# Kernel tuning notes

Measured on AMD Instinct MI355X. Metric: run time of the kernel, lower is better.

The kernel has to match this reference:

```python
import jax, jax.numpy as jnp
import numpy as np

N_NODES = 100000
N_EDGES = 1600000
HIDDEN = 256
CONV_OUT = 128
OUT = 2


def setup_inputs() -> dict:
    key = jax.random.key(0)
    k1, k2, k3, k4, k5, k6, k7 = jax.random.split(key, 7)
    x = jax.random.normal(k1, (N_NODES, HIDDEN), dtype=jnp.float32)
    edge_index = jax.random.randint(k2, (2, N_EDGES), 0, N_NODES, dtype=jnp.int64)
    edge_weight = jax.random.uniform(k3, (N_EDGES,), dtype=jnp.float32)
    # GCNConv parameters (lin: hidden->128, bias added after aggregation)
    W1 = jax.random.normal(k4, (HIDDEN, CONV_OUT), dtype=jnp.float32) / np.sqrt(HIDDEN)
    b1 = jnp.zeros((CONV_OUT,), dtype=jnp.float32)
    # head Linear(128, out_channels)
    W2 = jax.random.normal(k5, (CONV_OUT, OUT), dtype=jnp.float32) / np.sqrt(CONV_OUT)
    b2 = jax.random.normal(k6, (OUT,), dtype=jnp.float32) * 0.01
    return {"x": x, "edge_index": edge_index, "edge_weight": edge_weight,
            "W1": W1, "b1": b1, "W2": W2, "b2": b2}


def reference(x, edge_index, edge_weight, W1, b1, W2, b2):
    # GCNConv (use_weights=True branch, no relu), dropout in eval mode (identity), then Linear.
    N = x.shape[0]
    src, dst = edge_index[0], edge_index[1]
    # add self-loops with weight 1 (PyG default fill_value=1.0)
    loop = jnp.arange(N, dtype=src.dtype)
    src = jnp.concatenate([src, loop])
    dst = jnp.concatenate([dst, loop])
    w = jnp.concatenate([edge_weight, jnp.ones((N,), dtype=edge_weight.dtype)])
    # symmetric normalization: norm = d^{-1/2}[src] * w * d^{-1/2}[dst]
    deg = jax.ops.segment_sum(w, dst, num_segments=N)
    dinv = jnp.where(deg > 0, jax.lax.rsqrt(deg), 0.0)
    norm = dinv[src] * w * dinv[dst]
    # transform then gather-scatter aggregate
    h = x @ W1                                   # [N, 128]
    msgs = norm[:, None] * h[src]                # [E+N, 128]
    agg = jax.ops.segment_sum(msgs, dst, num_segments=N) + b1  # [N, 128]
    return agg @ W2 + b2                         # [N, out_channels]
```

## Files before the change

### kernel.cpp

```cpp
#include <hip/hip_runtime.h>

#define N_NODES 100000
#define N_EDGES 1600000
#define HIDDEN 256

#define BSH 7
#define BNODES 128
#define NB 782
#define NPB 256
#define EPB 6250
#define SLOTS 32
#define NZB 1563


__global__ __launch_bounds__(1024) void k_place(
        const int* __restrict__ ei, const float* __restrict__ ew,
        const float* __restrict__ W1, const float* __restrict__ b1,
        const float* __restrict__ W2, const float* __restrict__ b2,
        int* __restrict__ cnt, uint2* __restrict__ rec,
        float* __restrict__ W12, float* __restrict__ cvec) {
    const int tid = threadIdx.x, bid = blockIdx.x;
    if (bid == NPB) {
        if (tid < HIDDEN) {
            const float4* w1r = (const float4*)(W1 + (size_t)tid * 128);
            float a0 = 0.f, a1 = 0.f;
#pragma unroll 8
            for (int k4 = 0; k4 < 32; ++k4) {
                float4 v = w1r[k4];
                a0 += v.x * W2[8 * k4 + 0]; a1 += v.x * W2[8 * k4 + 1];
                a0 += v.y * W2[8 * k4 + 2]; a1 += v.y * W2[8 * k4 + 3];
                a0 += v.z * W2[8 * k4 + 4]; a1 += v.z * W2[8 * k4 + 5];
                a0 += v.w * W2[8 * k4 + 6]; a1 += v.w * W2[8 * k4 + 7];
            }
            W12[2 * tid] = a0; W12[2 * tid + 1] = a1;
            if (tid < 2) {
                float acc = b2[tid];
                for (int k = 0; k < 128; ++k) acc += b1[k] * W2[2 * k + tid];
                cvec[tid] = acc;
            }
        }
        return;
    }
    __shared__ int cursor[NB];
    for (int i = tid; i < NB; i += 1024) cursor[i] = 0;
    __syncthreads();
    const int e0 = bid * EPB, e1 = e0 + EPB;
    for (int e = e0 + tid; e < e1; e += 1024) {
        int d = ei[N_EDGES + e];
        int s = ei[e];
        float wv = ew[e];
        int bk = ((unsigned)d) >> BSH;
        int pos = atomicAdd(&cursor[bk], 1);
        if (pos < SLOTS)
            rec[((size_t)bk * NPB + bid) * SLOTS + pos] =
                make_uint2((unsigned)s | ((unsigned)(d & (BNODES - 1)) << 17),
                           __float_as_uint(wv));
    }
    __syncthreads();
    for (int i = tid; i < NB; i += 1024)
        cnt[(size_t)i * NPB + bid] = min(cursor[i], SLOTS);
}

__global__ __launch_bounds__(256) void k_zdeg(
        const float* __restrict__ x, const float* __restrict__ W12,
        const uint2* __restrict__ rec, const int* __restrict__ cnt,
        float* __restrict__ z, float* __restrict__ dinv) {
    __shared__ float acc[BNODES];
    const int tid = threadIdx.x, bid = blockIdx.x;
    if (bid < NZB) {
        const int lane = tid & 63;
        const int sub  = lane & 15;
        const int nid  = lane >> 4;
        float w0r[16], w1r[16];
#pragma unroll
        for (int j = 0; j < 16; ++j) {
            float2 wp = ((const float2*)W12)[sub * 16 + j];
            w0r[j] = wp.x; w1r[j] = wp.y;
        }
        const int base = bid * 64 + (tid >> 6) * 16;
#pragma unroll
        for (int k = 0; k < 4; ++k) {
            const int node = base + k * 4 + nid;
            if (node < N_NODES) {
                const float* xp = x + (size_t)node * HIDDEN + sub * 16;
                float xa[16];
                *(float4*)(xa + 0)  = *(const float4*)(xp + 0);
                *(float4*)(xa + 4)  = *(const float4*)(xp + 4);
                *(float4*)(xa + 8)  = *(const float4*)(xp + 8);
                *(float4*)(xa + 12) = *(const float4*)(xp + 12);
                float a0 = 0.f, a1 = 0.f;
#pragma unroll
                for (int j = 0; j < 16; ++j) {
                    a0 += xa[j] * w0r[j];
                    a1 += xa[j] * w1r[j];
                }
#pragma unroll
                for (int m = 1; m <= 8; m <<= 1) {
                    a0 += __shfl_xor(a0, m, 64);
                    a1 += __shfl_xor(a1, m, 64);
                }
                if (sub == 0) ((float2*)z)[node] = make_float2(a0, a1);
            }
        }
    } else {
        const int b = bid - NZB;
        if (tid < BNODES) acc[tid] = 1.0f;
        __syncthreads();
        const int n = cnt[(size_t)b * NPB + tid];
        const uint2* r = rec + ((size_t)b * NPB + tid) * SLOTS;
        int i = 0;
        for (; i + 2 <= n; i += 2) {
            uint4 q = *(const uint4*)(r + i);
            atomicAdd(&acc[q.x >> 17], __uint_as_float(q.y));
            atomicAdd(&acc[q.z >> 17], __uint_as_float(q.w));
        }
        if (i < n) {
            uint2 q = r[i];
            atomicAdd(&acc[q.x >> 17], __uint_as_float(q.y));
        }
        __syncthreads();
        if (tid < BNODES) {
            int node = b * BNODES + tid;
            if (node < N_NODES) dinv[node] = rsqrtf(acc[tid]);
        }
    }
}

__global__ __launch_bounds__(256) void k_gather(
        const uint2* __restrict__ rec, const int* __restrict__ cnt,
        const float* __restrict__ dinv, const float* __restrict__ z,
        const float* __restrict__ cvec, float2* __restrict__ out) {
    __shared__ float ax[BNODES], ay[BNODES];
    const int tid = threadIdx.x, b = blockIdx.x;
    if (tid < BNODES) { ax[tid] = 0.f; ay[tid] = 0.f; }
    __syncthreads();
    const int n = cnt[(size_t)b * NPB + tid];
    const uint2* r = rec + ((size_t)b * NPB + tid) * SLOTS;
    int i = 0;
    for (; i + 2 <= n; i += 2) {
        uint4 q = *(const uint4*)(r + i);
        int s0 = (int)(q.x & 0x1FFFFu), s1 = (int)(q.z & 0x1FFFFu);
        float di0 = dinv[s0], di1 = dinv[s1];
        float2 z0 = ((const float2*)z)[s0];
        float2 z1 = ((const float2*)z)[s1];
        float nw0 = di0 * __uint_as_float(q.y);
        float nw1 = di1 * __uint_as_float(q.w);
        int d0 = (int)(q.x >> 17), d1 = (int)(q.z >> 17);
        atomicAdd(&ax[d0], nw0 * z0.x);
        atomicAdd(&ay[d0], nw0 * z0.y);
        atomicAdd(&ax[d1], nw1 * z1.x);
        atomicAdd(&ay[d1], nw1 * z1.y);
    }
    if (i < n) {
        uint2 q = r[i];
        int s = (int)(q.x & 0x1FFFFu);
        float nw = dinv[s] * __uint_as_float(q.y);
        float2 zv = ((const float2*)z)[s];
        int dl = (int)(q.x >> 17);
        atomicAdd(&ax[dl], nw * zv.x);
        atomicAdd(&ay[dl], nw * zv.y);
    }
    __syncthreads();
    if (tid < BNODES) {
        int node = b * BNODES + tid;
        if (node < N_NODES) {
            float di = dinv[node];
            float2 zv = ((const float2*)z)[node];
            out[node] = make_float2(di * ax[tid] + di * di * zv.x + cvec[0],
                                    di * ay[tid] + di * di * zv.y + cvec[1]);
        }
    }
}

extern "C" void kernel_launch(void* const* d_in, const int* in_sizes, int n_in,
                              void* d_out, int out_size, void* d_ws, size_t ws_size,
                              hipStream_t stream) {
    const float* x  = (const float*)d_in[0];
    const int*   ei = (const int*)d_in[1];
    const float* ew = (const float*)d_in[2];
    const float* W1 = (const float*)d_in[3];
    const float* b1 = (const float*)d_in[4];
    const float* W2 = (const float*)d_in[5];
    const float* b2 = (const float*)d_in[6];
    float2* out = (float2*)d_out;

    char* ws = (char*)d_ws;
    uint2*  rec  = (uint2*)ws;           size_t off = (size_t)NB * NPB * SLOTS * 8;
    int*    cnt  = (int*)(ws + off);     off += (size_t)NB * NPB * 4;
    float*  dinv = (float*)(ws + off);   off += (size_t)N_NODES * 4;
    float*  z    = (float*)(ws + off);   off += (size_t)N_NODES * 8;
    float*  W12  = (float*)(ws + off);   off += HIDDEN * 2 * 4;
    float*  cvec = (float*)(ws + off);   off += 16;

    k_place <<<NPB + 1, 1024, 0, stream>>>(ei, ew, W1, b1, W2, b2, cnt, rec, W12, cvec);
    k_zdeg  <<<NZB + NB, 256, 0, stream>>>(x, W12, rec, cnt, z, dinv);
    k_gather<<<NB, 256, 0, stream>>>(rec, cnt, dinv, z, cvec, out);
}
```

Before: 78.59 us.

## Compute node projection with one thread per node and LDS-staged weights

The x·W12 projection switches from 16 lanes cooperating on each node (with shuffle reductions) to one thread per node. Each thread reads its whole 256-float row while the 256×2 combined weights sit in shared memory. This removes the cross-lane shuffles and cuts the number of projection blocks from 1563 to 391. In exchange, each wave-wide load now touches 64 rows 1 KB apart, so global loads of x are no longer coalesced and depend on cache reuse across loop iterations.

Result: slower. 85.34 us (+8.6%).

```diff
diff --git a/kernel.cpp b/kernel.cpp
--- a/kernel.cpp
+++ b/kernel.cpp
@@ -10,7 +10,7 @@
 #define NPB 256
 #define EPB 6250
 #define SLOTS 32
-#define NZB 1563
+#define NZT 391
 
 
 __global__ __launch_bounds__(1024) void k_place(
@@ -65,45 +65,31 @@
         const float* __restrict__ x, const float* __restrict__ W12,
         const uint2* __restrict__ rec, const int* __restrict__ cnt,
         float* __restrict__ z, float* __restrict__ dinv) {
+    __shared__ float lw0[HIDDEN], lw1[HIDDEN];
     __shared__ float acc[BNODES];
     const int tid = threadIdx.x, bid = blockIdx.x;
-    if (bid < NZB) {
-        const int lane = tid & 63;
-        const int sub  = lane & 15;
-        const int nid  = lane >> 4;
-        float w0r[16], w1r[16];
-#pragma unroll
-        for (int j = 0; j < 16; ++j) {
-            float2 wp = ((const float2*)W12)[sub * 16 + j];
-            w0r[j] = wp.x; w1r[j] = wp.y;
-        }
-        const int base = bid * 64 + (tid >> 6) * 16;
-#pragma unroll
-        for (int k = 0; k < 4; ++k) {
-            const int node = base + k * 4 + nid;
-            if (node < N_NODES) {
-                const float* xp = x + (size_t)node * HIDDEN + sub * 16;
-                float xa[16];
-                *(float4*)(xa + 0)  = *(const float4*)(xp + 0);
-                *(float4*)(xa + 4)  = *(const float4*)(xp + 4);
-                *(float4*)(xa + 8)  = *(const float4*)(xp + 8);
-                *(float4*)(xa + 12) = *(const float4*)(xp + 12);
-                float a0 = 0.f, a1 = 0.f;
-#pragma unroll
-                for (int j = 0; j < 16; ++j) {
-                    a0 += xa[j] * w0r[j];
-                    a1 += xa[j] * w1r[j];
-                }
-#pragma unroll
-                for (int m = 1; m <= 8; m <<= 1) {
-                    a0 += __shfl_xor(a0, m, 64);
-                    a1 += __shfl_xor(a1, m, 64);
-                }
-                if (sub == 0) ((float2*)z)[node] = make_float2(a0, a1);
+    if (bid < NZT) {
+        float2 wp = ((const float2*)W12)[tid];
+        lw0[tid] = wp.x; lw1[tid] = wp.y;
+        __syncthreads();
+        const int node = bid * 256 + tid;
+        if (node < N_NODES) {
+            const float4* xp = (const float4*)(x + (size_t)node * HIDDEN);
+            const float4* w0q = (const float4*)lw0;
+            const float4* w1q = (const float4*)lw1;
+            float a0 = 0.f, a1 = 0.f;
+#pragma unroll 8
+            for (int j = 0; j < 64; ++j) {
+                float4 v = xp[j];
+                float4 wa = w0q[j];
+                float4 wb = w1q[j];
+                a0 += v.x * wa.x + v.y * wa.y + v.z * wa.z + v.w * wa.w;
+                a1 += v.x * wb.x + v.y * wb.y + v.z * wb.z + v.w * wb.w;
             }
+            ((float2*)z)[node] = make_float2(a0, a1);
         }
     } else {
-        const int b = bid - NZB;
+        const int b = bid - NZT;
         if (tid < BNODES) acc[tid] = 1.0f;
         __syncthreads();
         const int n = cnt[(size_t)b * NPB + tid];
@@ -193,6 +179,6 @@
     float*  cvec = (float*)(ws + off);   off += 16;
 
     k_place <<<NPB + 1, 1024, 0, stream>>>(ei, ew, W1, b1, W2, b2, cnt, rec, W12, cvec);
-    k_zdeg  <<<NZB + NB, 256, 0, stream>>>(x, W12, rec, cnt, z, dinv);
+    k_zdeg  <<<NZT + NB, 256, 0, stream>>>(x, W12, rec, cnt, z, dinv);
     k_gather<<<NB, 256, 0, stream>>>(rec, cnt, dinv, z, cvec, out);
 }
```

## Stage x rows into LDS via direct global-to-LDS loads for z projection

Applied to the files above, without the earlier changes.

Rewrites the x·W12 projection so each wave copies 8 full rows of x into shared memory using global_load_lds (direct global-to-LDS DMA), then computes dot products from LDS with 8 lanes per node. W12 is stored as two separate column vectors for float4 loads, and the block count doubles because each block now covers 32 nodes. The aim is fully coalesced 1KB row loads with more bytes in flight. The cost is 32KB of LDS per block, which may limit occupancy, and the node bounds check is gone, which is only safe because 100000 divides evenly by 32.

After: 78.82 us. Within noise of the previous version (+0.3%).

```diff
diff --git a/kernel.cpp b/kernel.cpp
--- a/kernel.cpp
+++ b/kernel.cpp
@@ -10,7 +10,7 @@
 #define NPB 256
 #define EPB 6250
 #define SLOTS 32
-#define NZB 1563
+#define NZB 3125
 
 
 __global__ __launch_bounds__(1024) void k_place(
@@ -32,7 +32,8 @@
                 a0 += v.z * W2[8 * k4 + 4]; a1 += v.z * W2[8 * k4 + 5];
                 a0 += v.w * W2[8 * k4 + 6]; a1 += v.w * W2[8 * k4 + 7];
             }
-            W12[2 * tid] = a0; W12[2 * tid + 1] = a1;
+            W12[tid] = a0;
+            W12[HIDDEN + tid] = a1;
             if (tid < 2) {
                 float acc = b2[tid];
                 for (int k = 0; k < 128; ++k) acc += b1[k] * W2[2 * k + tid];
@@ -65,43 +66,43 @@
         const float* __restrict__ x, const float* __restrict__ W12,
         const uint2* __restrict__ rec, const int* __restrict__ cnt,
         float* __restrict__ z, float* __restrict__ dinv) {
+    __shared__ float tile[4][8][HIDDEN];
     __shared__ float acc[BNODES];
     const int tid = threadIdx.x, bid = blockIdx.x;
     if (bid < NZB) {
+        const int wv   = tid >> 6;
         const int lane = tid & 63;
-        const int sub  = lane & 15;
-        const int nid  = lane >> 4;
-        float w0r[16], w1r[16];
+        const int sub  = lane & 7;
+        const int nl   = lane >> 3;
+        float4 wa[8], wb[8];
 #pragma unroll
-        for (int j = 0; j < 16; ++j) {
-            float2 wp = ((const float2*)W12)[sub * 16 + j];
-            w0r[j] = wp.x; w1r[j] = wp.y;
+        for (int j = 0; j < 8; ++j) {
+            wa[j] = *(const float4*)(W12 + (sub + 8 * j) * 4);
+            wb[j] = *(const float4*)(W12 + HIDDEN + (sub + 8 * j) * 4);
         }
-        const int base = bid * 64 + (tid >> 6) * 16;
+        const int rowbase = bid * 32 + wv * 8;
 #pragma unroll
-        for (int k = 0; k < 4; ++k) {
-            const int node = base + k * 4 + nid;
-            if (node < N_NODES) {
-                const float* xp = x + (size_t)node * HIDDEN + sub * 16;
-                float xa[16];
-                *(float4*)(xa + 0)  = *(const float4*)(xp + 0);
-                *(float4*)(xa + 4)  = *(const float4*)(xp + 4);
-                *(float4*)(xa + 8)  = *(const float4*)(xp + 8);
-                *(float4*)(xa + 12) = *(const float4*)(xp + 12);
-                float a0 = 0.f, a1 = 0.f;
+        for (int j = 0; j < 8; ++j) {
+            const float* gsrc = x + (size_t)(rowbase + j) * HIDDEN + lane * 4;
+            __builtin_amdgcn_global_load_lds(
+                (const __attribute__((address_space(1))) void*)gsrc,
+                (__attribute__((address_space(3))) void*)&tile[wv][j][0],
+                16, 0, 0);
+        }
+        asm volatile("s_waitcnt vmcnt(0)" ::: "memory");
+        float a0 = 0.f, a1 = 0.f;
 #pragma unroll
-                for (int j = 0; j < 16; ++j) {
-                    a0 += xa[j] * w0r[j];
-                    a1 += xa[j] * w1r[j];
-                }
+        for (int j = 0; j < 8; ++j) {
+            float4 v = *(const float4*)&tile[wv][nl][(sub + 8 * j) * 4];
+            a0 += v.x * wa[j].x + v.y * wa[j].y + v.z * wa[j].z + v.w * wa[j].w;
+            a1 += v.x * wb[j].x + v.y * wb[j].y + v.z * wb[j].z + v.w * wb[j].w;
+        }
 #pragma unroll
-                for (int m = 1; m <= 8; m <<= 1) {
-                    a0 += __shfl_xor(a0, m, 64);
-                    a1 += __shfl_xor(a1, m, 64);
-                }
-                if (sub == 0) ((float2*)z)[node] = make_float2(a0, a1);
-            }
+        for (int m = 1; m <= 4; m <<= 1) {
+            a0 += __shfl_xor(a0, m, 64);
+            a1 += __shfl_xor(a1, m, 64);
         }
+        if (sub == 0) ((float2*)z)[rowbase + nl] = make_float2(a0, a1);
     } else {
         const int b = bid - NZB;
         if (tid < BNODES) acc[tid] = 1.0f;
```
